# Optimization experiments

Measured on AMD Instinct MI355X. Metric: run time of the kernel, lower is better.

Reference implementation:

```python
import jax, jax.numpy as jnp
import numpy as np


def _block_diag(blocks):
    """blocks: [K, m, n] -> dense block-diagonal [K*m, K*n] (vectorized scatter)."""
    K, m, n = blocks.shape
    out = jnp.zeros((K * m, K * n), blocks.dtype)
    r = jnp.arange(K)[:, None, None] * m + jnp.arange(m)[None, :, None]
    c = jnp.arange(K)[:, None, None] * n + jnp.arange(n)[None, None, :]
    return out.at[r, c].set(blocks)


def setup_inputs() -> dict:
    key = jax.random.key(0)
    k0, k1, k2, k3, k4 = jax.random.split(key, 5)
    n_state, n_input, T = 32, 16, 64
    n_all = n_state + n_input
    A = jax.random.normal(k0, (n_state, n_state), jnp.float32) * 0.3
    B = jax.random.normal(k1, (n_state, n_input), jnp.float32)
    M = jax.random.normal(k2, (T, n_all, n_all), jnp.float32)
    # symmetric PSD per-step cost blocks so the KKT matrix is invertible
    C = jnp.einsum('tij,tkj->tik', M, M) / n_all + 0.1 * jnp.eye(n_all, dtype=jnp.float32)
    c = jax.random.normal(k3, (T, n_all), jnp.float32)
    x0 = jax.random.normal(k4, (n_state,), jnp.float32)
    return {"A": A, "B": B, "C": C, "c": c, "T": T, "x0": x0}


def reference(A, B, C, c, T, x0):
    n_state = A.shape[0]
    n_input = B.shape[1]
    n_all = n_state + n_input

    # cost_mat = block_diag(C_0, ..., C_{T-1})  -> [n_all*T, n_all*T]
    cost_mat = _block_diag(C)

    # dynamics constraint matrix [n_state*T, n_all*T]
    AB = jnp.concatenate((A, B), axis=1)  # [n_state, n_all]
    AB_bd = _block_diag(jnp.broadcast_to(AB, (T - 1, n_state, n_all)) + jnp.zeros((T - 1, 1, 1), A.dtype))
    dynamics = jnp.zeros((n_state * T, n_all * T), A.dtype)
    dynamics = dynamics.at[:n_state, :n_state].set(jnp.eye(n_state, dtype=A.dtype))
    dynamics = dynamics.at[n_state:n_state * T, :n_all * (T - 1)].set(AB_bd)
    # -I coupling: rows n_state*t + i, cols n_all*t + i for t = 1..T-1
    rows = n_state * jnp.arange(1, T)[:, None] + jnp.arange(n_state)[None, :]
    cols = n_all * jnp.arange(1, T)[:, None] + jnp.arange(n_state)[None, :]
    dynamics = dynamics.at[rows, cols].set(-1.0)

    zero_mat = jnp.zeros((n_state * T, n_state * T), A.dtype)
    full_mat = jnp.block([[cost_mat, dynamics.T], [dynamics, zero_mat]])

    sol = jnp.zeros(n_all * T + n_state * T, A.dtype)
    sol = sol.at[n_all * T:n_all * T + n_state].set(x0)

    tau_mu = jnp.linalg.solve(full_mat, sol[:, None])[:, 0]
    tau_star = tau_mu[:n_all * T]
    mu_star = tau_mu[n_all * T:]
    return (tau_star, mu_star)
```

## Files before the change

### kernel.cpp

```cpp
#include <hip/hip_runtime.h>

#define NS 32
#define NI 16
#define NA 48
#define TT 64
#define HT 32
#define CSZ (NA * NA)

__launch_bounds__(256, 1)
__global__ void lqr_fast(const float* __restrict__ Ag,
                         const float* __restrict__ Bg,
                         const float* __restrict__ Cg,
                         const float* __restrict__ x0g,
                         float* __restrict__ out,
                         float* __restrict__ Kall,
                         float* __restrict__ Pall)
{
    __shared__ float  sXT[TT][NS];
    __shared__ float  sA[NS][33];
    __shared__ float  sB[NS][17];
    __shared__ double sP[NS][33];
    __shared__ double sPA[NS][33];
    __shared__ double sPB[NS][17];
    __shared__ double sHs[NI][33];
    __shared__ double sKt[NI][33];
    __shared__ double sGi[NI][17];
    __shared__ double sPp[NS][33];
    __shared__ double sx[2][NS];
    __shared__ double su[NI];

    const int tid  = threadIdx.x;
    const int wid  = tid >> 6, lane = tid & 63;
    const int pi   = tid >> 3, pj0 = (tid & 7) * 4, pb0 = (tid & 7) * 2;
    const int ki   = tid >> 4, kj0 = (tid & 15) * 2;

    for (int idx = tid; idx < NS * NS; idx += 256) {
        sA[idx >> 5][idx & 31] = Ag[idx];
        sP[idx >> 5][idx & 31] = 0.0;
    }
    for (int idx = tid; idx < NS * NI; idx += 256)
        sB[idx >> 4][idx & 15] = Bg[idx];
    __syncthreads();

    for (int t = TT - 1; t >= 0; --t) {
        const float* Ct = Cg + t * CSZ;

        {
            double a0 = 0, a1 = 0, a2 = 0, a3 = 0, b0 = 0, b1 = 0;
            for (int k = 0; k < NS; ++k) {
                const double p = sP[pi][k];
                a0 += p * (double)sA[k][pj0 + 0]; a1 += p * (double)sA[k][pj0 + 1];
                a2 += p * (double)sA[k][pj0 + 2]; a3 += p * (double)sA[k][pj0 + 3];
                b0 += p * (double)sB[k][pb0 + 0]; b1 += p * (double)sB[k][pb0 + 1];
            }
            sPA[pi][pj0 + 0] = a0; sPA[pi][pj0 + 1] = a1;
            sPA[pi][pj0 + 2] = a2; sPA[pi][pj0 + 3] = a3;
            sPB[pi][pb0 + 0] = b0; sPB[pi][pb0 + 1] = b1;
        }
        __syncthreads();

        if (wid == 0) {
            const int ri = lane & 15, cg = lane >> 4, jb = cg * 4;
            double g0 = (double)Ct[(NS + ri) * NA + NS + jb + 0];
            double g1 = (double)Ct[(NS + ri) * NA + NS + jb + 1];
            double g2 = (double)Ct[(NS + ri) * NA + NS + jb + 2];
            double g3 = (double)Ct[(NS + ri) * NA + NS + jb + 3];
            for (int k = 0; k < NS; ++k) {
                const double b = (double)sB[k][ri];
                g0 += b * sPB[k][jb + 0]; g1 += b * sPB[k][jb + 1];
                g2 += b * sPB[k][jb + 2]; g3 += b * sPB[k][jb + 3];
            }
#pragma unroll
            for (int k = 0; k < NI; ++k) {
                const double myslot = ((k & 3) == 0) ? g0 : ((k & 3) == 1) ? g1
                                     : ((k & 3) == 2) ? g2 : g3;
                const int    plv  = k + ((k >> 2) << 4);
                const double piv  = __shfl(myslot, plv, 64);
                const double cv   = __shfl(myslot, ri + ((k >> 2) << 4), 64);
                const double pr0  = __shfl(g0, k + (cg << 4), 64);
                const double pr1  = __shfl(g1, k + (cg << 4), 64);
                const double pr2  = __shfl(g2, k + (cg << 4), 64);
                const double pr3  = __shfl(g3, k + (cg << 4), 64);
                const double ip   = 1.0 / piv;
                const bool   rk   = (ri == k);
                g0 = rk ? ((jb + 0 == k) ? ip : pr0 * ip)
                        : ((jb + 0 == k) ? -cv * ip : g0 - cv * pr0 * ip);
                g1 = rk ? ((jb + 1 == k) ? ip : pr1 * ip)
                        : ((jb + 1 == k) ? -cv * ip : g1 - cv * pr1 * ip);
                g2 = rk ? ((jb + 2 == k) ? ip : pr2 * ip)
                        : ((jb + 2 == k) ? -cv * ip : g2 - cv * pr2 * ip);
                g3 = rk ? ((jb + 3 == k) ? ip : pr3 * ip)
                        : ((jb + 3 == k) ? -cv * ip : g3 - cv * pr3 * ip);
            }
            sGi[ri][jb + 0] = g0; sGi[ri][jb + 1] = g1;
            sGi[ri][jb + 2] = g2; sGi[ri][jb + 3] = g3;
        } else {
            const int e0 = tid - 64;
            for (int e = e0; e < NI * NS; e += 192) {
                const int i = e >> 5, j = e & 31;
                double acc = (double)Ct[j * NA + NS + i];
                for (int k = 0; k < NS; ++k) acc += (double)sB[k][i] * sPA[k][j];
                sHs[i][j] = acc;
            }
            for (int e = e0; e < NS * NS; e += 192) {
                const int i = e >> 5, j = e & 31;
                double acc = (double)Ct[i * NA + j];
                for (int k = 0; k < NS; ++k) acc += (double)sA[k][i] * sPA[k][j];
                sPp[i][j] = acc;
            }
        }
        __syncthreads();

        {
            double a0 = 0, a1 = 0;
            for (int k = 0; k < NI; ++k) {
                const double g = sGi[ki][k];
                a0 += g * sHs[k][kj0 + 0];
                a1 += g * sHs[k][kj0 + 1];
            }
            sKt[ki][kj0 + 0] = a0; sKt[ki][kj0 + 1] = a1;
            Kall[t * NI * NS + ki * NS + kj0 + 0] = (float)a0;
            Kall[t * NI * NS + ki * NS + kj0 + 1] = (float)a1;
        }
        __syncthreads();

        {
            double a0 = sPp[pi][pj0 + 0], a1 = sPp[pi][pj0 + 1];
            double a2 = sPp[pi][pj0 + 2], a3 = sPp[pi][pj0 + 3];
            for (int k = 0; k < NI; ++k) {
                const double h = sHs[k][pi];
                a0 -= h * sKt[k][pj0 + 0]; a1 -= h * sKt[k][pj0 + 1];
                a2 -= h * sKt[k][pj0 + 2]; a3 -= h * sKt[k][pj0 + 3];
            }
            double b0 = sPp[pj0 + 0][pi], b1 = sPp[pj0 + 1][pi];
            double b2 = sPp[pj0 + 2][pi], b3 = sPp[pj0 + 3][pi];
            for (int k = 0; k < NI; ++k) {
                const double hk = sKt[k][pi];
                b0 -= sHs[k][pj0 + 0] * hk; b1 -= sHs[k][pj0 + 1] * hk;
                b2 -= sHs[k][pj0 + 2] * hk; b3 -= sHs[k][pj0 + 3] * hk;
            }
            const double r0 = 0.5 * (a0 + b0), r1 = 0.5 * (a1 + b1);
            const double r2 = 0.5 * (a2 + b2), r3 = 0.5 * (a3 + b3);
            sP[pi][pj0 + 0] = r0; sP[pi][pj0 + 1] = r1;
            sP[pi][pj0 + 2] = r2; sP[pi][pj0 + 3] = r3;
            float* Pt = Pall + t * NS * NS + pi * NS + pj0;
            Pt[0] = (float)r0; Pt[1] = (float)r1; Pt[2] = (float)r2; Pt[3] = (float)r3;
        }
        __syncthreads();
    }

    if (tid < NS) sx[0][tid] = (double)x0g[tid];
    __syncthreads();
    int cur = 0;
    for (int t = 0; t < TT; ++t) {
        if (tid < NS) {
            const float xv = (float)sx[cur][tid];
            sXT[t][tid] = xv;
            out[t * NA + tid] = xv;
        } else if (tid >= 64 && tid < 64 + NI) {
            const int i = tid - 64;
            const float* Kt = Kall + t * NI * NS + i * NS;
            double acc = 0.0;
            for (int k = 0; k < NS; ++k) acc += (double)Kt[k] * sx[cur][k];
            su[i] = -acc;
            out[t * NA + NS + i] = (float)(-acc);
        }
        __syncthreads();
        if (t < TT - 1) {
            if (tid < NS) {
                double acc = 0.0;
                for (int k = 0; k < NS; ++k) acc += (double)sA[tid][k] * sx[cur][k];
                for (int k = 0; k < NI; ++k) acc += (double)sB[tid][k] * su[k];
                sx[cur ^ 1][tid] = acc;
            }
            __syncthreads();
            cur ^= 1;
        }
    }
    __syncthreads();

    for (int e = tid; e < TT * NS; e += 256) {
        const int t = e >> 5, i = e & 31;
        const float* Pt = Pall + t * NS * NS + i * NS;
        double acc = 0.0;
        for (int k = 0; k < NS; ++k) acc += (double)Pt[k] * (double)sXT[t][k];
        if (t == 0) acc = -acc;
        out[NA * TT + t * NS + i] = (float)acc;
    }
}

__launch_bounds__(256, 1)
__global__ void lqr_kernel_fb(const float* __restrict__ Ag,
                              const float* __restrict__ Bg,
                              const float* __restrict__ Cg,
                              const float* __restrict__ x0g,
                              float* __restrict__ out)
{
    __shared__ float  sKh[HT][NI][NS];
    __shared__ float  sXT[TT][NS];
    __shared__ double sA[NS][NS];
    __shared__ double sB[NS][NI];
    __shared__ double sP[NS][NS];
    __shared__ double sPA[NS][NS];
    __shared__ double sPB[NS][NI];
    __shared__ double sHs[NI][NS];
    __shared__ double sKt[NI][NS];
    __shared__ double sGi[NI][NI];
    __shared__ double sPp[NS][NS];
    __shared__ double sx[2][NS];
    __shared__ double su[NI];

    const int tid  = threadIdx.x;
    const int wid  = tid >> 6, lane = tid & 63;
    const int pi   = tid >> 3, pj0 = (tid & 7) * 4, pb0 = (tid & 7) * 2;
    const int ki   = tid >> 4, kj0 = (tid & 15) * 2;

    for (int idx = tid; idx < NS * NS; idx += 256) sA[idx >> 5][idx & 31] = (double)Ag[idx];
    for (int idx = tid; idx < NS * NI; idx += 256) sB[idx >> 4][idx & 15] = (double)Bg[idx];
    __syncthreads();

    auto step = [&](int t, bool storeK, int kbase, bool emitMu) {
        const float* Ct = Cg + t * NA * NA;
        {
            double a0 = 0, a1 = 0, a2 = 0, a3 = 0, b0 = 0, b1 = 0;
            for (int k = 0; k < NS; ++k) {
                const double p = sP[pi][k];
                a0 += p * sA[k][pj0 + 0]; a1 += p * sA[k][pj0 + 1];
                a2 += p * sA[k][pj0 + 2]; a3 += p * sA[k][pj0 + 3];
                b0 += p * sB[k][pb0 + 0]; b1 += p * sB[k][pb0 + 1];
            }
            sPA[pi][pj0 + 0] = a0; sPA[pi][pj0 + 1] = a1;
            sPA[pi][pj0 + 2] = a2; sPA[pi][pj0 + 3] = a3;
            sPB[pi][pb0 + 0] = b0; sPB[pi][pb0 + 1] = b1;
        }
        __syncthreads();
        if (wid == 0) {
            const int ri = lane & 15, cg = lane >> 4, jb = cg * 4;
            double g0 = (double)Ct[(NS + ri) * NA + NS + jb + 0];
            double g1 = (double)Ct[(NS + ri) * NA + NS + jb + 1];
            double g2 = (double)Ct[(NS + ri) * NA + NS + jb + 2];
            double g3 = (double)Ct[(NS + ri) * NA + NS + jb + 3];
            for (int k = 0; k < NS; ++k) {
                const double b = sB[k][ri];
                g0 += b * sPB[k][jb + 0]; g1 += b * sPB[k][jb + 1];
                g2 += b * sPB[k][jb + 2]; g3 += b * sPB[k][jb + 3];
            }
#pragma unroll
            for (int k = 0; k < NI; ++k) {
                const double myslot = ((k & 3) == 0) ? g0 : ((k & 3) == 1) ? g1
                                     : ((k & 3) == 2) ? g2 : g3;
                const int    plv  = k + ((k >> 2) << 4);
                const double piv  = __shfl(myslot, plv, 64);
                const double cv   = __shfl(myslot, ri + ((k >> 2) << 4), 64);
                const double pr0  = __shfl(g0, k + (cg << 4), 64);
                const double pr1  = __shfl(g1, k + (cg << 4), 64);
                const double pr2  = __shfl(g2, k + (cg << 4), 64);
                const double pr3  = __shfl(g3, k + (cg << 4), 64);
                const double ip   = 1.0 / piv;
                const bool   rk   = (ri == k);
                g0 = rk ? ((jb + 0 == k) ? ip : pr0 * ip)
                        : ((jb + 0 == k) ? -cv * ip : g0 - cv * pr0 * ip);
                g1 = rk ? ((jb + 1 == k) ? ip : pr1 * ip)
                        : ((jb + 1 == k) ? -cv * ip : g1 - cv * pr1 * ip);
                g2 = rk ? ((jb + 2 == k) ? ip : pr2 * ip)
                        : ((jb + 2 == k) ? -cv * ip : g2 - cv * pr2 * ip);
                g3 = rk ? ((jb + 3 == k) ? ip : pr3 * ip)
                        : ((jb + 3 == k) ? -cv * ip : g3 - cv * pr3 * ip);
            }
            sGi[ri][jb + 0] = g0; sGi[ri][jb + 1] = g1;
            sGi[ri][jb + 2] = g2; sGi[ri][jb + 3] = g3;
        } else {
            const int e0 = tid - 64;
            for (int e = e0; e < NI * NS; e += 192) {
                const int i = e >> 5, j = e & 31;
                double acc = (double)Ct[j * NA + NS + i];
                for (int k = 0; k < NS; ++k) acc += sB[k][i] * sPA[k][j];
                sHs[i][j] = acc;
            }
            for (int e = e0; e < NS * NS; e += 192) {
                const int i = e >> 5, j = e & 31;
                double acc = (double)Ct[i * NA + j];
                for (int k = 0; k < NS; ++k) acc += sA[k][i] * sPA[k][j];
                sPp[i][j] = acc;
            }
        }
        __syncthreads();
        {
            double a0 = 0, a1 = 0;
            for (int k = 0; k < NI; ++k) {
                const double g = sGi[ki][k];
                a0 += g * sHs[k][kj0 + 0];
                a1 += g * sHs[k][kj0 + 1];
            }
            sKt[ki][kj0 + 0] = a0; sKt[ki][kj0 + 1] = a1;
            if (storeK) {
                sKh[t - kbase][ki][kj0 + 0] = (float)a0;
                sKh[t - kbase][ki][kj0 + 1] = (float)a1;
            }
        }
        __syncthreads();
        {
            double a0 = sPp[pi][pj0 + 0], a1 = sPp[pi][pj0 + 1];
            double a2 = sPp[pi][pj0 + 2], a3 = sPp[pi][pj0 + 3];
            for (int k = 0; k < NI; ++k) {
                const double h = sHs[k][pi];
                a0 -= h * sKt[k][pj0 + 0]; a1 -= h * sKt[k][pj0 + 1];
                a2 -= h * sKt[k][pj0 + 2]; a3 -= h * sKt[k][pj0 + 3];
            }
            double b0 = sPp[pj0 + 0][pi], b1 = sPp[pj0 + 1][pi];
            double b2 = sPp[pj0 + 2][pi], b3 = sPp[pj0 + 3][pi];
            for (int k = 0; k < NI; ++k) {
                const double hk = sKt[k][pi];
                b0 -= sHs[k][pj0 + 0] * hk; b1 -= sHs[k][pj0 + 1] * hk;
                b2 -= sHs[k][pj0 + 2] * hk; b3 -= sHs[k][pj0 + 3] * hk;
            }
            sP[pi][pj0 + 0] = 0.5 * (a0 + b0); sP[pi][pj0 + 1] = 0.5 * (a1 + b1);
            sP[pi][pj0 + 2] = 0.5 * (a2 + b2); sP[pi][pj0 + 3] = 0.5 * (a3 + b3);
        }
        __syncthreads();
        if (emitMu && tid < NS) {
            double acc = 0.0;
            for (int k = 0; k < NS; ++k) acc += sP[tid][k] * (double)sXT[t][k];
            if (t == 0) acc = -acc;
            out[NA * TT + t * NS + tid] = (float)acc;
        }
    };

    auto sweep = [&](int tlo, int klo, int khi, bool emitMu) {
        for (int idx = tid; idx < NS * NS; idx += 256) sP[idx >> 5][idx & 31] = 0.0;
        __syncthreads();
        for (int t = TT - 1; t >= tlo; --t)
            step(t, (t >= klo && t < khi), klo, emitMu);
    };

    int cur = 0;
    auto forward = [&](int t0, int t1, int kbase) {
        for (int t = t0; t < t1; ++t) {
            if (tid < NS) {
                const float xv = (float)sx[cur][tid];
                sXT[t][tid] = xv;
                out[t * NA + tid] = xv;
            } else if (tid >= 64 && tid < 64 + NI) {
                const int i = tid - 64;
                double acc = 0.0;
                for (int k = 0; k < NS; ++k)
                    acc += (double)sKh[t - kbase][i][k] * sx[cur][k];
                su[i] = -acc;
                out[t * NA + NS + i] = (float)(-acc);
            }
            __syncthreads();
            if (t < TT - 1) {
                if (tid < NS) {
                    double acc = 0.0;
                    for (int k = 0; k < NS; ++k) acc += sA[tid][k] * sx[cur][k];
                    for (int k = 0; k < NI; ++k) acc += sB[tid][k] * su[k];
                    sx[cur ^ 1][tid] = acc;
                }
                __syncthreads();
                cur ^= 1;
            }
        }
    };

    sweep(0, 0, HT, false);
    if (tid < NS) sx[0][tid] = (double)x0g[tid];
    __syncthreads();
    forward(0, HT, 0);
    sweep(HT, HT, TT, false);
    forward(HT, TT, HT);
    sweep(0, 0, 0, true);
}

extern "C" void kernel_launch(void* const* d_in, const int* in_sizes, int n_in,
                              void* d_out, int out_size, void* d_ws, size_t ws_size,
                              hipStream_t stream) {
    const float *A = nullptr, *B = nullptr, *C = nullptr, *x0 = nullptr;
    for (int i = 0; i < n_in; ++i) {
        switch (in_sizes[i]) {
            case 1024:   A  = (const float*)d_in[i]; break;
            case 512:    B  = (const float*)d_in[i]; break;
            case 147456: C  = (const float*)d_in[i]; break;
            case 32:     x0 = (const float*)d_in[i]; break;
            default: break;
        }
    }
    if (!A || !B || !C || !x0) {
        A  = (const float*)d_in[0];
        B  = (const float*)d_in[1];
        C  = (const float*)d_in[2];
        x0 = (const float*)d_in[5];
    }

    const size_t need = (size_t)(TT * NI * NS + TT * NS * NS) * sizeof(float);
    if (d_ws != nullptr && ws_size >= need) {
        float* Kall = (float*)d_ws;
        float* Pall = Kall + TT * NI * NS;
        lqr_fast<<<1, 256, 0, stream>>>(A, B, C, x0, (float*)d_out, Kall, Pall);
    } else {
        lqr_kernel_fb<<<1, 256, 0, stream>>>(A, B, C, x0, (float*)d_out);
    }
}
```

Before: 564.2 us.

## Exploit symmetry of P in Riccati update and precompute thread index maps

The Riccati update now computes only the upper triangle of the symmetric P' and P matrices (528 entries) and mirrors the results, replacing the earlier full-matrix computation that averaged with the transpose. The loops over H and P' elements are unrolled into fixed per-thread register accumulators with index mappings decoded once before the time loop. This cuts double-precision FMA work per step on the serial backward recursion. In exchange it drops the explicit symmetrization, which may change rounding slightly, and the mirrored writes can cause shared-memory bank conflicts.

```diff
diff --git a/kernel.cpp b/kernel.cpp
--- a/kernel.cpp
+++ b/kernel.cpp
@@ -6,6 +6,13 @@
 #define TT 64
 #define HT 32
 #define CSZ (NA * NA)
+#define NTRI 528
+
+__device__ __forceinline__ void tri_decode(int e, int& i, int& j) {
+    int ii = 0, rem = e;
+    while (rem >= NS - ii) { rem -= NS - ii; ++ii; }
+    i = ii; j = ii + rem;
+}
 
 __launch_bounds__(256, 1)
 __global__ void lqr_fast(const float* __restrict__ Ag,
@@ -34,6 +41,25 @@
     const int pi   = tid >> 3, pj0 = (tid & 7) * 4, pb0 = (tid & 7) * 2;
     const int ki   = tid >> 4, kj0 = (tid & 15) * 2;
 
+    const int e0   = tid - 64;
+    const int hI0_ = (e0 >= 0) ? (e0 >> 5) : 0,        hJ0_ = (e0 >= 0) ? (e0 & 31) : 0;
+    const int hI1_ = (e0 >= 0) ? ((e0+192) >> 5) : 0,  hJ1_ = (e0 >= 0) ? ((e0+192) & 31) : 0;
+    const bool hasH2 = (e0 >= 0) && (e0 + 384 < 512);
+    const int hI2_ = hasH2 ? ((e0+384) >> 5) : 0,      hJ2_ = hasH2 ? ((e0+384) & 31) : 0;
+    int pI0_ = 0, pJ0_ = 0, pI1_ = 0, pJ1_ = 0, pI2_ = 0, pJ2_ = 0;
+    bool hasP2 = false;
+    if (e0 >= 0) {
+        tri_decode(e0, pI0_, pJ0_);
+        tri_decode(e0 + 192, pI1_, pJ1_);
+        hasP2 = (e0 + 384 < NTRI);
+        if (hasP2) tri_decode(e0 + 384, pI2_, pJ2_);
+    }
+    int fI0_, fJ0_, fI1_, fJ1_, fI2_ = 0, fJ2_ = 0;
+    tri_decode(tid, fI0_, fJ0_);
+    tri_decode(tid + 256, fI1_, fJ1_);
+    const bool hasF2 = (tid + 512 < NTRI);
+    if (hasF2) tri_decode(tid + 512, fI2_, fJ2_);
+
     for (int idx = tid; idx < NS * NS; idx += 256) {
         sA[idx >> 5][idx & 31] = Ag[idx];
         sP[idx >> 5][idx & 31] = 0.0;
@@ -95,19 +121,26 @@
             sGi[ri][jb + 0] = g0; sGi[ri][jb + 1] = g1;
             sGi[ri][jb + 2] = g2; sGi[ri][jb + 3] = g3;
         } else {
-            const int e0 = tid - 64;
-            for (int e = e0; e < NI * NS; e += 192) {
-                const int i = e >> 5, j = e & 31;
-                double acc = (double)Ct[j * NA + NS + i];
-                for (int k = 0; k < NS; ++k) acc += (double)sB[k][i] * sPA[k][j];
-                sHs[i][j] = acc;
-            }
-            for (int e = e0; e < NS * NS; e += 192) {
-                const int i = e >> 5, j = e & 31;
-                double acc = (double)Ct[i * NA + j];
-                for (int k = 0; k < NS; ++k) acc += (double)sA[k][i] * sPA[k][j];
-                sPp[i][j] = acc;
-            }
+            double h0 = (double)Ct[hJ0_ * NA + NS + hI0_];
+            double h1 = (double)Ct[hJ1_ * NA + NS + hI1_];
+            double h2 = hasH2 ? (double)Ct[hJ2_ * NA + NS + hI2_] : 0.0;
+            double q0 = (double)Ct[pI0_ * NA + pJ0_];
+            double q1 = (double)Ct[pI1_ * NA + pJ1_];
+            double q2 = hasP2 ? (double)Ct[pI2_ * NA + pJ2_] : 0.0;
+            for (int k = 0; k < NS; ++k) {
+                h0 += (double)sB[k][hI0_] * sPA[k][hJ0_];
+                h1 += (double)sB[k][hI1_] * sPA[k][hJ1_];
+                h2 += (double)sB[k][hI2_] * sPA[k][hJ2_];
+                q0 += (double)sA[k][pI0_] * sPA[k][pJ0_];
+                q1 += (double)sA[k][pI1_] * sPA[k][pJ1_];
+                q2 += (double)sA[k][pI2_] * sPA[k][pJ2_];
+            }
+            sHs[hI0_][hJ0_] = h0;
+            sHs[hI1_][hJ1_] = h1;
+            if (hasH2) sHs[hI2_][hJ2_] = h2;
+            sPp[pI0_][pJ0_] = q0; sPp[pJ0_][pI0_] = q0;
+            sPp[pI1_][pJ1_] = q1; sPp[pJ1_][pI1_] = q1;
+            if (hasP2) { sPp[pI2_][pJ2_] = q2; sPp[pJ2_][pI2_] = q2; }
         }
         __syncthreads();
 
@@ -125,26 +158,23 @@
         __syncthreads();
 
         {
-            double a0 = sPp[pi][pj0 + 0], a1 = sPp[pi][pj0 + 1];
-            double a2 = sPp[pi][pj0 + 2], a3 = sPp[pi][pj0 + 3];
-            for (int k = 0; k < NI; ++k) {
-                const double h = sHs[k][pi];
-                a0 -= h * sKt[k][pj0 + 0]; a1 -= h * sKt[k][pj0 + 1];
-                a2 -= h * sKt[k][pj0 + 2]; a3 -= h * sKt[k][pj0 + 3];
-            }
-            double b0 = sPp[pj0 + 0][pi], b1 = sPp[pj0 + 1][pi];
-            double b2 = sPp[pj0 + 2][pi], b3 = sPp[pj0 + 3][pi];
-            for (int k = 0; k < NI; ++k) {
-                const double hk = sKt[k][pi];
-                b0 -= sHs[k][pj0 + 0] * hk; b1 -= sHs[k][pj0 + 1] * hk;
-                b2 -= sHs[k][pj0 + 2] * hk; b3 -= sHs[k][pj0 + 3] * hk;
-            }
-            const double r0 = 0.5 * (a0 + b0), r1 = 0.5 * (a1 + b1);
-            const double r2 = 0.5 * (a2 + b2), r3 = 0.5 * (a3 + b3);
-            sP[pi][pj0 + 0] = r0; sP[pi][pj0 + 1] = r1;
-            sP[pi][pj0 + 2] = r2; sP[pi][pj0 + 3] = r3;
-            float* Pt = Pall + t * NS * NS + pi * NS + pj0;
-            Pt[0] = (float)r0; Pt[1] = (float)r1; Pt[2] = (float)r2; Pt[3] = (float)r3;
+            double a0 = sPp[fI0_][fJ0_];
+            double a1 = sPp[fI1_][fJ1_];
+            double a2 = hasF2 ? sPp[fI2_][fJ2_] : 0.0;
+            for (int k = 0; k < NI; ++k) {
+                a0 -= sHs[k][fI0_] * sKt[k][fJ0_];
+                a1 -= sHs[k][fI1_] * sKt[k][fJ1_];
+                a2 -= sHs[k][fI2_] * sKt[k][fJ2_];
+            }
+            sP[fI0_][fJ0_] = a0; sP[fJ0_][fI0_] = a0;
+            sP[fI1_][fJ1_] = a1; sP[fJ1_][fI1_] = a1;
+            float* Pt = Pall + t * NS * NS;
+            Pt[fI0_ * NS + fJ0_] = (float)a0; Pt[fJ0_ * NS + fI0_] = (float)a0;
+            Pt[fI1_ * NS + fJ1_] = (float)a1; Pt[fJ1_ * NS + fI1_] = (float)a1;
+            if (hasF2) {
+                sP[fI2_][fJ2_] = a2; sP[fJ2_][fI2_] = a2;
+                Pt[fI2_ * NS + fJ2_] = (float)a2; Pt[fJ2_ * NS + fI2_] = (float)a2;
+            }
         }
         __syncthreads();
     }
```

Result: faster. 526.3 us (-6.7%).

## Exploit symmetry of Riccati P update and remap Hs/Pp work to 4-wide thread blocks

Applied to the files above, without the earlier changes.

Computes only the upper-triangular 4-wide blocks of the symmetric Pp and P matrices and mirrors them, instead of computing full matrices and symmetrizing by averaging. The Hs and Pp products are also reassigned from strided scalar loops to fixed per-thread 4-column register blocks, with some threads handling a second block. This roughly halves the arithmetic in the serial backward Riccati loop. In exchange it adds divergent branches and loses the explicit symmetrization, which may slightly change rounding.

```diff
diff --git a/kernel.cpp b/kernel.cpp
--- a/kernel.cpp
+++ b/kernel.cpp
@@ -6,6 +6,13 @@
 #define TT 64
 #define HT 32
 #define CSZ (NA * NA)
+#define NPB 144
+
+__device__ __forceinline__ void pblk_decode(int b, int& i, int& j0) {
+    int ii = 0, rem = b;
+    for (;;) { const int c = 8 - (ii >> 2); if (rem < c) break; rem -= c; ++ii; }
+    i = ii; j0 = ((ii >> 2) << 2) + rem * 4;
+}
 
 __launch_bounds__(256, 1)
 __global__ void lqr_fast(const float* __restrict__ Ag,
@@ -34,6 +41,18 @@
     const int pi   = tid >> 3, pj0 = (tid & 7) * 4, pb0 = (tid & 7) * 2;
     const int ki   = tid >> 4, kj0 = (tid & 15) * 2;
 
+    bool isHs0 = false, has1 = false;
+    int i0 = 0, j00 = 0, i1 = 0, j01 = 0;
+    if (tid >= 64) {
+        const int q = tid - 64;
+        if (q < 128) { isHs0 = true; i0 = q >> 3; j00 = (q & 7) * 4; }
+        else pblk_decode(q - 128, i0, j00);
+        if (q < 80) { has1 = true; pblk_decode(q + 64, i1, j01); }
+    }
+    int fi = 0, fj0 = 0;
+    const bool hasF = (tid < NPB);
+    if (hasF) pblk_decode(tid, fi, fj0);
+
     for (int idx = tid; idx < NS * NS; idx += 256) {
         sA[idx >> 5][idx & 31] = Ag[idx];
         sP[idx >> 5][idx & 31] = 0.0;
@@ -95,18 +114,55 @@
             sGi[ri][jb + 0] = g0; sGi[ri][jb + 1] = g1;
             sGi[ri][jb + 2] = g2; sGi[ri][jb + 3] = g3;
         } else {
-            const int e0 = tid - 64;
-            for (int e = e0; e < NI * NS; e += 192) {
-                const int i = e >> 5, j = e & 31;
-                double acc = (double)Ct[j * NA + NS + i];
-                for (int k = 0; k < NS; ++k) acc += (double)sB[k][i] * sPA[k][j];
-                sHs[i][j] = acc;
-            }
-            for (int e = e0; e < NS * NS; e += 192) {
-                const int i = e >> 5, j = e & 31;
-                double acc = (double)Ct[i * NA + j];
-                for (int k = 0; k < NS; ++k) acc += (double)sA[k][i] * sPA[k][j];
-                sPp[i][j] = acc;
+            const float* wp = isHs0 ? &sB[0][i0] : &sA[0][i0];
+            const int    ws = isHs0 ? 17 : 33;
+            double c0, c1, c2, c3;
+            if (isHs0) {
+                c0 = (double)Ct[(j00 + 0) * NA + NS + i0];
+                c1 = (double)Ct[(j00 + 1) * NA + NS + i0];
+                c2 = (double)Ct[(j00 + 2) * NA + NS + i0];
+                c3 = (double)Ct[(j00 + 3) * NA + NS + i0];
+            } else {
+                c0 = (double)Ct[i0 * NA + j00 + 0];
+                c1 = (double)Ct[i0 * NA + j00 + 1];
+                c2 = (double)Ct[i0 * NA + j00 + 2];
+                c3 = (double)Ct[i0 * NA + j00 + 3];
+            }
+            double d0 = 0, d1 = 0, d2 = 0, d3 = 0;
+            if (has1) {
+                d0 = (double)Ct[i1 * NA + j01 + 0];
+                d1 = (double)Ct[i1 * NA + j01 + 1];
+                d2 = (double)Ct[i1 * NA + j01 + 2];
+                d3 = (double)Ct[i1 * NA + j01 + 3];
+            }
+            for (int k = 0; k < NS; ++k) {
+                const double w0 = (double)wp[k * ws];
+                c0 += w0 * sPA[k][j00 + 0];
+                c1 += w0 * sPA[k][j00 + 1];
+                c2 += w0 * sPA[k][j00 + 2];
+                c3 += w0 * sPA[k][j00 + 3];
+                if (has1) {
+                    const double w1 = (double)sA[k][i1];
+                    d0 += w1 * sPA[k][j01 + 0];
+                    d1 += w1 * sPA[k][j01 + 1];
+                    d2 += w1 * sPA[k][j01 + 2];
+                    d3 += w1 * sPA[k][j01 + 3];
+                }
+            }
+            if (isHs0) {
+                sHs[i0][j00 + 0] = c0; sHs[i0][j00 + 1] = c1;
+                sHs[i0][j00 + 2] = c2; sHs[i0][j00 + 3] = c3;
+            } else {
+                if (j00 + 0 >= i0) { sPp[i0][j00 + 0] = c0; if (j00 + 0 > i0) sPp[j00 + 0][i0] = c0; }
+                if (j00 + 1 >= i0) { sPp[i0][j00 + 1] = c1; if (j00 + 1 > i0) sPp[j00 + 1][i0] = c1; }
+                if (j00 + 2 >= i0) { sPp[i0][j00 + 2] = c2; if (j00 + 2 > i0) sPp[j00 + 2][i0] = c2; }
+                if (j00 + 3 >= i0) { sPp[i0][j00 + 3] = c3; if (j00 + 3 > i0) sPp[j00 + 3][i0] = c3; }
+            }
+            if (has1) {
+                if (j01 + 0 >= i1) { sPp[i1][j01 + 0] = d0; if (j01 + 0 > i1) sPp[j01 + 0][i1] = d0; }
+                if (j01 + 1 >= i1) { sPp[i1][j01 + 1] = d1; if (j01 + 1 > i1) sPp[j01 + 1][i1] = d1; }
+                if (j01 + 2 >= i1) { sPp[i1][j01 + 2] = d2; if (j01 + 2 > i1) sPp[j01 + 2][i1] = d2; }
+                if (j01 + 3 >= i1) { sPp[i1][j01 + 3] = d3; if (j01 + 3 > i1) sPp[j01 + 3][i1] = d3; }
             }
         }
         __syncthreads();
@@ -124,27 +180,27 @@
         }
         __syncthreads();
 
-        {
-            double a0 = sPp[pi][pj0 + 0], a1 = sPp[pi][pj0 + 1];
-            double a2 = sPp[pi][pj0 + 2], a3 = sPp[pi][pj0 + 3];
-            for (int k = 0; k < NI; ++k) {
-                const double h = sHs[k][pi];
-                a0 -= h * sKt[k][pj0 + 0]; a1 -= h * sKt[k][pj0 + 1];
-                a2 -= h * sKt[k][pj0 + 2]; a3 -= h * sKt[k][pj0 + 3];
-            }
-            double b0 = sPp[pj0 + 0][pi], b1 = sPp[pj0 + 1][pi];
-            double b2 = sPp[pj0 + 2][pi], b3 = sPp[pj0 + 3][pi];
-            for (int k = 0; k < NI; ++k) {
-                const double hk = sKt[k][pi];
-                b0 -= sHs[k][pj0 + 0] * hk; b1 -= sHs[k][pj0 + 1] * hk;
-                b2 -= sHs[k][pj0 + 2] * hk; b3 -= sHs[k][pj0 + 3] * hk;
-            }
-            const double r0 = 0.5 * (a0 + b0), r1 = 0.5 * (a1 + b1);
-            const double r2 = 0.5 * (a2 + b2), r3 = 0.5 * (a3 + b3);
-            sP[pi][pj0 + 0] = r0; sP[pi][pj0 + 1] = r1;
-            sP[pi][pj0 + 2] = r2; sP[pi][pj0 + 3] = r3;
-            float* Pt = Pall + t * NS * NS + pi * NS + pj0;
-            Pt[0] = (float)r0; Pt[1] = (float)r1; Pt[2] = (float)r2; Pt[3] = (float)r3;
+        if (hasF) {
+            double a0 = sPp[fi][fj0 + 0];
+            double a1 = sPp[fi][fj0 + 1];
+            double a2 = sPp[fi][fj0 + 2];
+            double a3 = sPp[fi][fj0 + 3];
+            for (int k = 0; k < NI; ++k) {
+                const double h = sHs[k][fi];
+                a0 -= h * sKt[k][fj0 + 0];
+                a1 -= h * sKt[k][fj0 + 1];
+                a2 -= h * sKt[k][fj0 + 2];
+                a3 -= h * sKt[k][fj0 + 3];
+            }
+            float* Pt = Pall + t * NS * NS;
+            if (fj0 + 0 >= fi) { sP[fi][fj0 + 0] = a0; Pt[fi * NS + fj0 + 0] = (float)a0;
+                if (fj0 + 0 > fi) { sP[fj0 + 0][fi] = a0; Pt[(fj0 + 0) * NS + fi] = (float)a0; } }
+            if (fj0 + 1 >= fi) { sP[fi][fj0 + 1] = a1; Pt[fi * NS + fj0 + 1] = (float)a1;
+                if (fj0 + 1 > fi) { sP[fj0 + 1][fi] = a1; Pt[(fj0 + 1) * NS + fi] = (float)a1; } }
+            if (fj0 + 2 >= fi) { sP[fi][fj0 + 2] = a2; Pt[fi * NS + fj0 + 2] = (float)a2;
+                if (fj0 + 2 > fi) { sP[fj0 + 2][fi] = a2; Pt[(fj0 + 2) * NS + fi] = (float)a2; } }
+            if (fj0 + 3 >= fi) { sP[fi][fj0 + 3] = a3; Pt[fi * NS + fj0 + 3] = (float)a3;
+                if (fj0 + 3 > fi) { sP[fj0 + 3][fi] = a3; Pt[(fj0 + 3) * NS + fi] = (float)a3; } }
         }
         __syncthreads();
     }
```

After: 607.7 us. +7.7%, slower.
